# Kernel optimization log

Hardware: AMD Instinct MI355X
Metric: run time of the kernel (lower is better)

Reference implementation:

```python
import jax, jax.numpy as jnp
import numpy as np

D = 64
NEG = 0.01            # leakyrelu_neg_slope
X_CONN = 0.25         # x_connection_init
SKIP_H = 0.5          # skip_weight_h
SIGMAS = np.asarray(1.5 ** np.arange(15), np.float32)  # all_sigmas_dist

N_LIG, N_REC = 4096, 8192
E_LIG, E_REC = 65536, 262144
F_LIG, F_REC, NRBF = 15, 27, 15


def _lrelu(x):
    return jax.nn.leaky_relu(x, NEG)


def _ln(x, g, b, eps=1e-5):
    m = x.mean(-1, keepdims=True)
    v = ((x - m) ** 2).mean(-1, keepdims=True)
    return (x - m) * jax.lax.rsqrt(v + eps) * g + b


def _mlp2(x, w1, b1, g, bt, w2, b2):
    # nn.Sequential(Linear, Dropout(0), LeakyReLU, LayerNorm, Linear) in eval mode
    return _ln(_lrelu(x @ w1 + b1), g, bt) @ w2 + b2


def _coords_mlp(m, w1, b1, w2, b2):
    # nn.Sequential(Linear, Dropout(0), LeakyReLU, Linear(out,1))
    return _lrelu(m @ w1 + b1) @ w2 + b2  # [E, 1]


def _seg_mean(v, idx, n):
    # DGL fn.mean over incoming edges at destination nodes (0 for isolated nodes)
    s = jax.ops.segment_sum(v, idx, num_segments=n)
    c = jax.ops.segment_sum(jnp.ones(idx.shape, v.dtype), idx, num_segments=n)
    return s / jnp.maximum(c, 1.0)[:, None]


def setup_inputs() -> dict:
    key = jax.random.key(0)
    ks = iter(jax.random.split(key, 64))

    def n(shape, s=1.0):
        return jax.random.normal(next(ks), shape, jnp.float32) * s

    def lin(i, o):
        return n((i, o), 1.0 / float(np.sqrt(i)))

    zeros = lambda *s: jnp.zeros(s, jnp.float32)
    ones = lambda *s: jnp.ones(s, jnp.float32)

    d = {}
    d['coords_lig'] = n((N_LIG, 3))
    d['h_lig'] = n((N_LIG, D))
    d['orig_h_lig'] = n((N_LIG, D))
    d['orig_coords_lig'] = n((N_LIG, 3))
    d['coords_rec'] = n((N_REC, 3))
    d['h_rec'] = n((N_REC, D))
    d['orig_h_rec'] = n((N_REC, D))
    d['orig_coords_rec'] = n((N_REC, 3))
    d['lig_src'] = jax.random.randint(next(ks), (E_LIG,), 0, N_LIG)
    d['lig_dst'] = jax.random.randint(next(ks), (E_LIG,), 0, N_LIG)
    d['lig_efeat'] = n((E_LIG, F_LIG))
    d['rec_src'] = jax.random.randint(next(ks), (E_REC,), 0, N_REC)
    d['rec_dst'] = jax.random.randint(next(ks), (E_REC,), 0, N_REC)
    d['rec_efeat'] = n((E_REC, F_REC))
    d['mask'] = (jax.random.uniform(next(ks), (N_LIG, N_REC)) < 0.5).astype(jnp.float32)
    # ---- parameters ----
    d['lig_em_w1'], d['lig_em_b1'] = lin(2 * D + F_LIG + NRBF, D), zeros(D)
    d['lig_em_g'], d['lig_em_bt'] = ones(D), zeros(D)
    d['lig_em_w2'], d['lig_em_b2'] = lin(D, D), zeros(D)
    d['rec_em_w1'], d['rec_em_b1'] = lin(2 * D + F_REC + NRBF, D), zeros(D)
    d['rec_em_g'], d['rec_em_bt'] = ones(D), zeros(D)
    d['rec_em_w2'], d['rec_em_b2'] = lin(D, D), zeros(D)
    d['lig_cm_w1'], d['lig_cm_b1'] = lin(D, D), zeros(D)
    d['lig_cm_w2'], d['lig_cm_b2'] = lin(D, 1), zeros(1)
    d['rec_cm_w1'], d['rec_cm_b1'] = lin(D, D), zeros(D)
    d['rec_cm_w2'], d['rec_cm_b2'] = lin(D, 1), zeros(1)
    for nm in ['q_lig_w', 'k_lig_w', 'v_lig_w', 'q_rec_w', 'k_rec_w', 'v_rec_w']:
        d[nm] = lin(D, D)
    d['lig_nm_w1'], d['lig_nm_b1'] = lin(4 * D, D), zeros(D)
    d['lig_nm_g'], d['lig_nm_bt'] = ones(D), zeros(D)
    d['lig_nm_w2'], d['lig_nm_b2'] = lin(D, D), zeros(D)
    d['rec_nm_w1'], d['rec_nm_b1'] = lin(4 * D, D), zeros(D)
    d['rec_nm_g'], d['rec_nm_bt'] = ones(D), zeros(D)
    d['rec_nm_w2'], d['rec_nm_b2'] = lin(D, D), zeros(D)
    return d


def reference(coords_lig, h_lig, orig_h_lig, orig_coords_lig,
              coords_rec, h_rec, orig_h_rec, orig_coords_rec,
              lig_src, lig_dst, lig_efeat, rec_src, rec_dst, rec_efeat, mask,
              lig_em_w1, lig_em_b1, lig_em_g, lig_em_bt, lig_em_w2, lig_em_b2,
              rec_em_w1, rec_em_b1, rec_em_g, rec_em_bt, rec_em_w2, rec_em_b2,
              lig_cm_w1, lig_cm_b1, lig_cm_w2, lig_cm_b2,
              rec_cm_w1, rec_cm_b1, rec_cm_w2, rec_cm_b2,
              q_lig_w, k_lig_w, v_lig_w, q_rec_w, k_rec_w, v_rec_w,
              lig_nm_w1, lig_nm_b1, lig_nm_g, lig_nm_bt, lig_nm_w2, lig_nm_b2,
              rec_nm_w1, rec_nm_b1, rec_nm_g, rec_nm_bt, rec_nm_w2, rec_nm_b2):
    n_lig, n_rec = coords_lig.shape[0], coords_rec.shape[0]
    sig = jnp.asarray(SIGMAS, coords_lig.dtype)

    # --- ligand edge messages: x_rel = x_src - x_dst, multi-scale RBF of |x_rel|^2 ---
    xr_l = coords_lig[lig_src] - coords_lig[lig_dst]                       # [E_l, 3]
    rbf_l = jnp.exp(-jnp.sum(xr_l * xr_l, -1, keepdims=True) / sig)        # [E_l, 15]
    msg_l = _mlp2(jnp.concatenate([h_lig[lig_src], h_lig[lig_dst], lig_efeat, rbf_l], -1),
                  lig_em_w1, lig_em_b1, lig_em_g, lig_em_bt, lig_em_w2, lig_em_b2)

    # --- receptor edge messages (rec_square_distance_scale = 1) ---
    xr_r = coords_rec[rec_src] - coords_rec[rec_dst]
    rbf_r = jnp.exp(-jnp.sum(xr_r * xr_r, -1, keepdims=True) / sig)
    msg_r = _mlp2(jnp.concatenate([h_rec[rec_src], h_rec[rec_dst], rec_efeat, rbf_r], -1),
                  rec_em_w1, rec_em_b1, rec_em_g, rec_em_bt, rec_em_w2, rec_em_b2)

    # --- masked cross-graph attention (pre/post cross-msg norms are identity) ---
    q_l, k_l, v_l = _lrelu(h_lig @ q_lig_w), _lrelu(h_lig @ k_lig_w), h_lig @ v_lig_w
    q_r, k_r, v_r = _lrelu(h_rec @ q_rec_w), _lrelu(h_rec @ k_rec_w), h_rec @ v_rec_w
    s_lr = mask * (q_l @ k_r.T) - 1000.0 * (1.0 - mask)
    att_l = jax.nn.softmax(s_lr, axis=1) @ v_r                             # [N_l, D]
    mt = mask.T
    s_rl = mt * (q_r @ k_l.T) - 1000.0 * (1.0 - mt)
    att_r = jax.nn.softmax(s_rl, axis=1) @ v_l                             # [N_r, D]

    # --- equivariant coordinate update: mean_j phi_x(m_ij) * x_rel, + skip to orig ---
    coef_l = _coords_mlp(msg_l, lig_cm_w1, lig_cm_b1, lig_cm_w2, lig_cm_b2)
    x_lig = X_CONN * orig_coords_lig + (1.0 - X_CONN) * coords_lig + _seg_mean(xr_l * coef_l, lig_dst, n_lig)
    coef_r = _coords_mlp(msg_r, rec_cm_w1, rec_cm_b1, rec_cm_w2, rec_cm_b2)
    x_rec = X_CONN * orig_coords_rec + (1.0 - X_CONN) * coords_rec + _seg_mean(xr_r * coef_r, rec_dst, n_rec)

    # --- node feature update with skip (h_feats_dim == out_feats_dim) ---
    aggr_l = _seg_mean(msg_l, lig_dst, n_lig)
    h_lig_out = SKIP_H * _mlp2(jnp.concatenate([h_lig, aggr_l, att_l, orig_h_lig], -1),
                               lig_nm_w1, lig_nm_b1, lig_nm_g, lig_nm_bt, lig_nm_w2, lig_nm_b2) \
        + (1.0 - SKIP_H) * h_lig
    aggr_r = _seg_mean(msg_r, rec_dst, n_rec)
    h_rec_out = SKIP_H * _mlp2(jnp.concatenate([h_rec, aggr_r, att_r, orig_h_rec], -1),
                               rec_nm_w1, rec_nm_b1, rec_nm_g, rec_nm_bt, rec_nm_w2, rec_nm_b2) \
        + (1.0 - SKIP_H) * h_rec
    return x_lig, h_lig_out, x_rec, h_rec_out
```

## Files before the change

### kernel.cpp

```cpp
#include <hip/hip_runtime.h>
#include <hip/hip_bf16.h>

typedef __hip_bfloat16 bf16;
typedef __attribute__((ext_vector_type(8))) short bfrag8;
typedef __attribute__((ext_vector_type(4))) float f32x4;

#define N_LIG 4096
#define N_REC 8192
#define E_LIG 65536
#define E_REC 262144
#define F_LIGc 15
#define F_RECc 27

__device__ __forceinline__ float ldkv(const float* p, size_t i) { return p[i]; }
__device__ __forceinline__ float ldkv(const bf16* p, size_t i) { return __bfloat162float(p[i]); }
__device__ __forceinline__ short bfbits(float x) {
    bf16 b = __float2bfloat16(x);
    return *(short*)&b;
}
__device__ __forceinline__ unsigned short stg(const float* p, size_t i) {
    return (unsigned short)bfbits(p[i]);
}
__device__ __forceinline__ unsigned short stg(const bf16* p, size_t i) {
    return *(const unsigned short*)(p + i);
// ... 498 lines not shown
}

template <int MMODE>
__device__ __forceinline__ void attn_body(
    char* sbuf, int bid, int nb1,
    const float* __restrict__ h1, const float* __restrict__ qw1,
    const bf16* __restrict__ k1, const bf16* __restrict__ v1,
    const unsigned long long* __restrict__ mq1, const float* __restrict__ mf1, long mrs1, long mcs1,
    float* __restrict__ pO1, float* __restrict__ pM1, float* __restrict__ pL1,
    int nrows1, int ncols1, int nsplit1,
    const float* __restrict__ h2, const float* __restrict__ qw2,
    const bf16* __restrict__ k2, const bf16* __restrict__ v2,
    const unsigned long long* __restrict__ mq2, const float* __restrict__ mf2, long mrs2, long mcs2,
    float* __restrict__ pO2, float* __restrict__ pM2, float* __restrict__ pL2,
    int nrows2, int ncols2, int nsplit2)
{
    const float *h, *qw, *mf;
    const bf16 *kkp, *vvp;
    const unsigned long long* mq;
    long mrs, mcs;
    float *pO, *pM, *pL;
    int n_rows, n_cols, nsplit;
    if (bid < nb1) {
        h = h1; qw = qw1; kkp = k1; vvp = v1; mq = mq1; mf = mf1; mrs = mrs1; mcs = mcs1;
        pO = pO1; pM = pM1; pL = pL1; n_rows = nrows1; n_cols = ncols1; nsplit = nsplit1;
    } else {
        h = h2; qw = qw2; kkp = k2; vvp = v2; mq = mq2; mf = mf2; mrs = mrs2; mcs = mcs2;
        pO = pO2; pM = pM2; pL = pL2; n_rows = nrows2; n_cols = ncols2; nsplit = nsplit2;
        bid -= nb1;
    }

    unsigned short* sP = (unsigned short*)sbuf;
    unsigned short* sK = (unsigned short*)(sbuf + 8192);
    unsigned short* sV = (unsigned short*)(sbuf + 16384);
    uint2* mtq = (uint2*)(sbuf + 24576);
    unsigned char* mt = (unsigned char*)(sbuf + 24576);

    const int t  = threadIdx.x;
    const int wv = t >> 6;
    const int lm = t & 15;
    const int qd = (t & 63) >> 4;
    const int rb = bid / nsplit;
    const int sp = bid - rb * nsplit;
    const int r0 = rb * 64;
    const int cols_per = n_cols / nsplit;
    const int c_begin = sp * cols_per;

    const int cP = t >> 3, segP = (t & 7) * 8;

    #pragma unroll
    for (int u = 0; u < 2; ++u) {
        int rr = cP + 32 * u;
        const float* hp = h + (size_t)(r0 + rr) * 64 + segP;
        unsigned short tmp[8];
        #pragma unroll
        for (int j = 0; j < 8; ++j) tmp[j] = bfbits(hp[j]);
        *(uint4*)&sP[swz(rr, segP)] = *(uint4*)tmp;
        const float* qp = qw + (size_t)rr * 64 + segP;
        #pragma unroll
        for (int j = 0; j < 8; ++j) sK[swz(segP + j, rr)] = bfbits(qp[j]);
    }

    uint4 kreg[2], vreg[2];
    unsigned long long mregq = 0;
    kreg[0] = *(const uint4*)(kkp + (size_t)(c_begin + cP) * 64 + segP);
    kreg[1] = *(const uint4*)(kkp + (size_t)(c_begin + cP + 32) * 64 + segP);
    vreg[0] = *(const uint4*)(vvp + (size_t)(c_begin + cP) * 64 + segP);
    vreg[1] = *(const uint4*)(vvp + (size_t)(c_begin + cP + 32) * 64 + segP);
    if (MMODE == 0 && t < 64)
        mregq = mq[(size_t)(c_begin >> 6) * n_rows + r0 + t];
    __syncthreads();

    float qv[4][4];
    {
        bfrag8 a0 = *(const bfrag8*)&sP[swz(wv * 16 + lm, qd * 8)];
        bfrag8 a1 = *(const bfrag8*)&sP[swz(wv * 16 + lm, 32 + qd * 8)];
        #pragma unroll
        for (int ns = 0; ns < 4; ++ns) {
            f32x4 acc = {0.f, 0.f, 0.f, 0.f};
            bfrag8 b0 = *(const bfrag8*)&sK[swz(ns * 16 + lm, qd * 8)];
            bfrag8 b1 = *(const bfrag8*)&sK[swz(ns * 16 + lm, 32 + qd * 8)];
            acc = __builtin_amdgcn_mfma_f32_16x16x32_bf16(a0, b0, acc, 0, 0, 0);
            acc = __builtin_amdgcn_mfma_f32_16x16x32_bf16(a1, b1, acc, 0, 0, 0);
            #pragma unroll
            for (int r = 0; r < 4; ++r) {
                float v = acc[r];
                qv[ns][r] = v > 0.f ? v : 0.01f * v;
            }
        }
    }
    __syncthreads();

    #pragma unroll
    for (int ns = 0; ns < 4; ++ns)
        #pragma unroll
        for (int r = 0; r < 4; ++r)
            sP[swz(wv * 16 + qd * 4 + r, ns * 16 + lm)] = bfbits(qv[ns][r]);
    __syncthreads();
    bfrag8 aq0 = *(const bfrag8*)&sP[swz(wv * 16 + lm, qd * 8)];
    bfrag8 aq1 = *(const bfrag8*)&sP[swz(wv * 16 + lm, 32 + qd * 8)];

    float rm[4];
    #pragma unroll
    for (int r = 0; r < 4; ++r) rm[r] = -1e30f;
    f32x4 o[4];
    #pragma unroll
    for (int ds = 0; ds < 4; ++ds) o[ds] = (f32x4){0.f, 0.f, 0.f, 0.f};
    f32x4 osum = {0.f, 0.f, 0.f, 0.f};
    const short ONE = (short)0x3F80;
    const bfrag8 bones = {ONE, ONE, ONE, ONE, ONE, ONE, ONE, ONE};

    const int nt = cols_per / 64;
    for (int tile = 0; tile < nt; ++tile) {
        #pragma unroll
        for (int u = 0; u < 2; ++u) {
            int cc = cP + 32 * u;
            *(uint4*)&sK[swz(cc, segP)] = kreg[u];
            unsigned x0 = vreg[u].x, x1 = vreg[u].y, x2 = vreg[u].z, x3 = vreg[u].w;
            sV[swz(segP + 0, cc)] = (unsigned short)x0;
            sV[swz(segP + 1, cc)] = (unsigned short)(x0 >> 16);
            sV[swz(segP + 2, cc)] = (unsigned short)x1;
            sV[swz(segP + 3, cc)] = (unsigned short)(x1 >> 16);
            sV[swz(segP + 4, cc)] = (unsigned short)x2;
            sV[swz(segP + 5, cc)] = (unsigned short)(x2 >> 16);
            sV[swz(segP + 6, cc)] = (unsigned short)x3;
            sV[swz(segP + 7, cc)] = (unsigned short)(x3 >> 16);
        }
        if (MMODE == 0) {
            if (t < 64) mtq[t] = make_uint2((unsigned)mregq, (unsigned)(mregq >> 32));
        } else {
            int c0 = c_begin + tile * 64;
            #pragma unroll
            for (int u = 0; u < 16; ++u) {
                int i = t + 256 * u;
                int r = i >> 6, c = i & 63;
                mt[r * 80 + c] = (unsigned char)(
                    mf[(size_t)(r0 + r) * mrs + (size_t)(c0 + c) * mcs] != 0.f);
            }
        }
        __syncthreads();

        if (tile + 1 < nt) {
            int c0n = c_begin + (tile + 1) * 64;
            kreg[0] = *(const uint4*)(kkp + (size_t)(c0n + cP) * 64 + segP);
            kreg[1] = *(const uint4*)(kkp + (size_t)(c0n + cP + 32) * 64 + segP);
            vreg[0] = *(const uint4*)(vvp + (size_t)(c0n + cP) * 64 + segP);
            vreg[1] = *(const uint4*)(vvp + (size_t)(c0n + cP + 32) * 64 + segP);
            if (MMODE == 0 && t < 64)
                mregq = mq[(size_t)(c0n >> 6) * n_rows + r0 + t];
        }

        f32x4 s[4];
        #pragma unroll
        for (int ns = 0; ns < 4; ++ns) {
            f32x4 acc = {0.f, 0.f, 0.f, 0.f};
            bfrag8 b0 = *(const bfrag8*)&sK[swz(ns * 16 + lm, qd * 8)];
            bfrag8 b1 = *(const bfrag8*)&sK[swz(ns * 16 + lm, 32 + qd * 8)];
            acc = __builtin_amdgcn_mfma_f32_16x16x32_bf16(aq0, b0, acc, 0, 0, 0);
            acc = __builtin_amdgcn_mfma_f32_16x16x32_bf16(aq1, b1, acc, 0, 0, 0);
            s[ns] = acc;
        }

        float alpha[4];
        #pragma unroll
        for (int r = 0; r < 4; ++r) {
            int rloc = wv * 16 + qd * 4 + r;
            float v0, v1, v2, v3;
            if (MMODE == 0) {
                uint2 w = mtq[rloc];
                v0 = (w.x >> lm) & 1        ? s[0][r] : -1000.f;
                v1 = (w.x >> (16 + lm)) & 1 ? s[1][r] : -1000.f;
                v2 = (w.y >> lm) & 1        ? s[2][r] : -1000.f;
                v3 = (w.y >> (16 + lm)) & 1 ? s[3][r] : -1000.f;
            } else {
                v0 = mt[rloc * 80 +  0 + lm] ? s[0][r] : -1000.f;
                v1 = mt[rloc * 80 + 16 + lm] ? s[1][r] : -1000.f;
                v2 = mt[rloc * 80 + 32 + lm] ? s[2][r] : -1000.f;
                v3 = mt[rloc * 80 + 48 + lm] ? s[3][r] : -1000.f;
            }
            float mx = quad_max(fmaxf(fmaxf(v0, v1), fmaxf(v2, v3)));
            float mn = fmaxf(rm[r], mx);
            float al = __expf(rm[r] - mn);
            rm[r] = mn; alpha[r] = al;
            float p0 = __expf(v0 - mn), p1 = __expf(v1 - mn);
            float p2 = __expf(v2 - mn), p3 = __expf(v3 - mn);
            sP[swz(rloc,  0 + lm)] = bfbits(p0);
            sP[swz(rloc, 16 + lm)] = bfbits(p1);
            sP[swz(rloc, 32 + lm)] = bfbits(p2);
            sP[swz(rloc, 48 + lm)] = bfbits(p3);
            osum[r] *= al;
        }
        #pragma unroll
        for (int ds = 0; ds < 4; ++ds)
            #pragma unroll
            for (int r = 0; r < 4; ++r) o[ds][r] *= alpha[r];

        __builtin_amdgcn_wave_barrier();
        asm volatile("" ::: "memory");

        {
            bfrag8 a0 = *(const bfrag8*)&sP[swz(wv * 16 + lm, qd * 8)];
            bfrag8 a1 = *(const bfrag8*)&sP[swz(wv * 16 + lm, 32 + qd * 8)];
            #pragma unroll
            for (int ds = 0; ds < 4; ++ds) {
                bfrag8 b0 = *(const bfrag8*)&sV[swz(ds * 16 + lm, qd * 8)];
                bfrag8 b1 = *(const bfrag8*)&sV[swz(ds * 16 + lm, 32 + qd * 8)];
                o[ds] = __builtin_amdgcn_mfma_f32_16x16x32_bf16(a0, b0, o[ds], 0, 0, 0);
                o[ds] = __builtin_amdgcn_mfma_f32_16x16x32_bf16(a1, b1, o[ds], 0, 0, 0);
            }
            osum = __builtin_amdgcn_mfma_f32_16x16x32_bf16(a0, bones, osum, 0, 0, 0);
            osum = __builtin_amdgcn_mfma_f32_16x16x32_bf16(a1, bones, osum, 0, 0, 0);
        }
        __syncthreads();
    }

    #pragma unroll
    for (int ds = 0; ds < 4; ++ds)
        #pragma unroll
        for (int r = 0; r < 4; ++r) {
            int row = r0 + wv * 16 + qd * 4 + r;
            pO[((size_t)sp * n_rows + row) * 64 + ds * 16 + lm] = o[ds][r];
        }
    if (lm == 0) {
        #pragma unroll
        for (int r = 0; r < 4; ++r) {
            int row = r0 + wv * 16 + qd * 4 + r;
            pM[(size_t)sp * n_rows + row] = rm[r];
            pL[(size_t)sp * n_rows + row] = osum[r];
        }
    }
}

__global__ __launch_bounds__(256, 4) void mega_kernel(
    int nb1,
    const float* h1, const float* qw1, const bf16* k1, const bf16* v1,
    const unsigned long long* mq1, float* pO1, float* pM1, float* pL1,
    int nrows1, int ncols1, int ns1,
    const float* h2, const float* qw2, const bf16* k2, const bf16* v2,
    const unsigned long long* mq2, float* pO2, float* pM2, float* pL2,
    int nrows2, int ncols2, int ns2,
    const int* ordR, const float* coordsR, const bf16* hR,
    const int* srcR, const int* dstR, const bf16* efR,
    const unsigned short* w1pR, const float* b1R, const float* gR, const float* btR,
    const unsigned short* w2pR, const float* b2R,
    const unsigned short* c1pR, const float* cb1R, const float* cw2R, const float* cb2R,
    float* aggrR, float* xaccR,
    const int* ordL, const float* coordsL, const bf16* hL,
    const int* srcL, const int* dstL, const bf16* efL,
    const unsigned short* w1pL, const float* b1L, const float* gL, const float* btL,
    const unsigned short* w2pL, const float* b2L,
    const unsigned short* c1pL, const float* cb1L, const float* cw2L, const float* cb2L,
    float* aggrL, float* xaccL)
{
    __shared__ __align__(16) char sbuf[31232];
    int bid = blockIdx.x;
    const int nbAtt = (N_LIG / 64) * ns1 + (N_REC / 64) * ns2;
    if (bid < nbAtt) {
        attn_body<0>(sbuf, bid, nb1,
            h1, qw1, k1, v1, mq1, (const float*)0, 0L, 0L, pO1, pM1, pL1, nrows1, ncols1, ns1,
            h2, qw2, k2, v2, mq2, (const float*)0, 0L, 0L, pO2, pM2, pL2, nrows2, ncols2, ns2);
    } else {
        int eid = bid - nbAtt;
        if (eid < E_REC / 64)
            edge_body<F_RECc, 6, bf16>(sbuf, eid, ordR, coordsR, hR, srcR, dstR, efR,
                w1pR, b1R, gR, btR, w2pR, b2R, c1pR, cb1R, cw2R, cb2R, aggrR, xaccR);
        else
            edge_body<F_LIGc, 5, bf16>(sbuf, eid - E_REC / 64, ordL, coordsL, hL, srcL, dstL, efL,
                w1pL, b1L, gL, btL, w2pL, b2L, c1pL, cb1L, cw2L, cb2L, aggrL, xaccL);
    }
}

template <int F, int K1S>
__global__ __launch_bounds__(256, 4) void edge_mfma_f(
    const int* order, const float* coords, const float* h,
    const int* src, const int* dst, const float* efeat,
    const unsigned short* w1p, const float* b1, const float* g, const float* bt,
    const unsigned short* w2p, const float* b2,
    const unsigned short* c1p, const float* cb1, const float* cw2, const float* cb2,
    float* aggr, float* xacc)
{
    __shared__ __align__(16) char sbuf[64 * (K1S * 32 + 8) * 2 + 5632];
    edge_body<F, K1S, float>(sbuf, blockIdx.x, order, coords, h, src, dst, efeat,
        w1p, b1, g, bt, w2p, b2, c1p, cb1, cw2, cb2, aggr, xacc);
}

__global__ __launch_bounds__(256, 4) void attn_f32mask(
    int nb1,
    const float* h1, const float* qw1, const bf16* k1, const bf16* v1,
    const float* mf1, long mrs1, long mcs1,
    float* pO1, float* pM1, float* pL1, int nrows1, int ncols1, int ns1,
    const float* h2, const float* qw2, const bf16* k2, const bf16* v2,
    const float* mf2, long mrs2, long mcs2,
    float* pO2, float* pM2, float* pL2, int nrows2, int ncols2, int ns2)
{
    __shared__ __align__(16) char sbuf[29696];
    attn_body<1>(sbuf, blockIdx.x, nb1,
        h1, qw1, k1, v1, (const unsigned long long*)0, mf1, mrs1, mcs1,
        pO1, pM1, pL1, nrows1, ncols1, ns1,
        h2, qw2, k2, v2, (const unsigned long long*)0, mf2, mrs2, mcs2,
        pO2, pM2, pL2, nrows2, ncols2, ns2);
}

__global__ __launch_bounds__(256, 3) void node_mfma(
    int nbl, int nbn,
    const float* h1, const float* __restrict__ aggr1, const int* __restrict__ cnt1,
    const float* att1, const float* __restrict__ origh1,
    const unsigned short* __restrict__ w1pa, const float* __restrict__ b1a,
    const float* __restrict__ ga, const float* __restrict__ bta,
    const unsigned short* __restrict__ w2pa, const float* __restrict__ b2a, float* out1,
    const float* h2, const float* __restrict__ aggr2, const int* __restrict__ cnt2,
    const float* att2, const float* __restrict__ origh2,
    const unsigned short* __restrict__ w1pb, const float* __restrict__ b1b,
    const float* __restrict__ gb, const float* __restrict__ btb,
    const unsigned short* __restrict__ w2pb, const float* __restrict__ b2b, float* out2,
    const float* __restrict__ ocl, const float* __restrict__ ccl,
    const float* __restrict__ xaccl, float* __restrict__ outxl,
    const float* __restrict__ ocr, const float* __restrict__ ccr,
    const float* __restrict__ xaccr, float* __restrict__ outxr)
{
    if ((int)blockIdx.x >= nbn) {
        int i = (blockIdx.x - nbn) * 256 + threadIdx.x;
        if (i < N_LIG * 3) {
            int node = i / 3;
            float invc = 1.f / fmaxf((float)cnt1[node], 1.f);
            outxl[i] = 0.25f * ocl[i] + 0.75f * ccl[i] + xaccl[i] * invc;
        } else {
            i -= N_LIG * 3;
            if (i < N_REC * 3) {
                int node = i / 3;
                float invc = 1.f / fmaxf((float)cnt2[node], 1.f);
                outxr[i] = 0.25f * ocr[i] + 0.75f * ccr[i] + xaccr[i] * invc;
            }
        }
        return;
    }

    const float *h, *aggr, *att, *orig_h, *b1, *g, *bt, *b2;
    const unsigned short *w1p, *w2p;
    const int* cnt;
    float* h_out;
    int n0;
    if ((int)blockIdx.x < nbl) {
        h = h1; aggr = aggr1; cnt = cnt1; att = att1; orig_h = origh1;
        w1p = w1pa; b1 = b1a; g = ga; bt = bta; w2p = w2pa; b2 = b2a; h_out = out1;
        n0 = blockIdx.x * 64;
    } else {
        h = h2; aggr = aggr2; cnt = cnt2; att = att2; orig_h = origh2;
        w1p = w1pb; b1 = b1b; g = gb; bt = btb; w2p = w2pb; b2 = b2b; h_out = out2;
        n0 = (blockIdx.x - nbl) * 64;
    }

    constexpr int KP = 264;
    __shared__ __align__(16) char smem[64 * KP * 2];
    __shared__ __align__(16) unsigned short h1b[64 * 72];
    __shared__ float sums[256], sums2[256];
    __shared__ float stat_m[64], stat_r[64];
    __shared__ float invc_s[64];
    unsigned short* xb  = (unsigned short*)smem;
    float*          h1f = (float*)smem;

    const int t  = threadIdx.x;
    const int wv = t >> 6;
    const int L  = t & 63;
    const int lm = t & 15;
    const int qd = (t & 63) >> 4;
    const int n  = wv * 16 + lm;

    bfrag8 w1f[8], w2f[2];
    #pragma unroll
    for (int kk = 0; kk < 8; ++kk)
        w1f[kk] = *(const bfrag8*)&w1p[((size_t)(kk * 4 + wv) * 64 + L) * 8];
    #pragma unroll
    for (int kk = 0; kk < 2; ++kk)
        w2f[kk] = *(const bfrag8*)&w2p[((size_t)(kk * 4 + wv) * 64 + L) * 8];
    const float b1n = b1[n], b2n = b2[n];

    if (t < 64) invc_s[t] = 1.f / fmaxf((float)cnt[n0 + t], 1.f);
    __syncthreads();

    #pragma unroll
    for (int it = 0; it < 8; ++it) {
        int idx = t + 256 * it;
        int e   = idx >> 5;
        int c   = idx & 31;
        int arr = c >> 3, ch = (c & 7) * 8;
        const float* sp;
        if      (arr == 0) sp = h      + (size_t)(n0 + e) * 64 + ch;
        else if (arr == 1) sp = aggr   + (size_t)(n0 + e) * 64 + ch;
        else if (arr == 2) sp = att    + (size_t)(n0 + e) * 64 + ch;
        else               sp = orig_h + (size_t)(n0 + e) * 64 + ch;
        float4 a = *(const float4*)sp;
        float4 b = *(const float4*)(sp + 4);
        float s = (arr == 1) ? invc_s[e] : 1.f;
        unsigned short tmp[8] = {
            (unsigned short)bfbits(a.x * s), (unsigned short)bfbits(a.y * s),
            (unsigned short)bfbits(a.z * s), (unsigned short)bfbits(a.w * s),
            (unsigned short)bfbits(b.x * s), (unsigned short)bfbits(b.y * s),
            (unsigned short)bfbits(b.z * s), (unsigned short)bfbits(b.w * s)};
        *(uint4*)&xb[e * KP + arr * 64 + ch] = *(uint4*)tmp;
    }
    __syncthreads();

    f32x4 acc1[4];
    #pragma unroll
    for (int m = 0; m < 4; ++m) {
        f32x4 acc = {0.f, 0.f, 0.f, 0.f};
        #pragma unroll
        for (int kk = 0; kk < 8; ++kk) {
            bfrag8 a = *(const bfrag8*)&xb[(m * 16 + lm) * KP + kk * 32 + qd * 8];
            acc = __builtin_amdgcn_mfma_f32_16x16x32_bf16(a, w1f[kk], acc, 0, 0, 0);
        }
        acc1[m] = acc;
    }
    __syncthreads();
    #pragma unroll
    for (int m = 0; m < 4; ++m)
        #pragma unroll
        for (int r = 0; r < 4; ++r) {
            int mr = m * 16 + qd * 4 + r;
            float v = acc1[m][r] + b1n;
            v = v > 0.f ? v : 0.01f * v;
            h1f[mr * 68 + n] = v;
        }
    __syncthreads();

    {
        int e = t >> 2, seg = (t & 3) * 16;
        float s1 = 0.f, s2 = 0.f;
        #pragma unroll
        for (int j = 0; j < 16; ++j) {
            float v = h1f[e * 68 + seg + j];
            s1 += v; s2 += v * v;
        }
        sums[t] = s1; sums2[t] = s2;
    }
    __syncthreads();
    if (t < 64) {
        float s1 = sums[4 * t] + sums[4 * t + 1] + sums[4 * t + 2] + sums[4 * t + 3];
        float s2 = sums2[4 * t] + sums2[4 * t + 1] + sums2[4 * t + 2] + sums2[4 * t + 3];
        float mean = s1 * (1.f / 64.f);
        float var = s2 * (1.f / 64.f) - mean * mean;
        stat_m[t] = mean;
        stat_r[t] = rsqrtf(fmaxf(var, 0.f) + 1e-5f);
    }
    __syncthreads();
    for (int idx = t; idx < 4096; idx += 256) {
        int e = idx >> 6, j = idx & 63;
        float v = (h1f[e * 68 + j] - stat_m[e]) * stat_r[e] * g[j] + bt[j];
        h1b[e * 72 + j] = bfbits(v);
    }
    __syncthreads();

    #pragma unroll
    for (int m = 0; m < 4; ++m) {
        f32x4 acc = {0.f, 0.f, 0.f, 0.f};
        #pragma unroll
        for (int kk = 0; kk < 2; ++kk) {
            bfrag8 a = *(const bfrag8*)&h1b[(m * 16 + lm) * 72 + kk * 32 + qd * 8];
            acc = __builtin_amdgcn_mfma_f32_16x16x32_bf16(a, w2f[kk], acc, 0, 0, 0);
        }
        #pragma unroll
        for (int r = 0; r < 4; ++r) {
            int row = n0 + m * 16 + qd * 4 + r;
            float o = acc[r] + b2n;
            float hv = h[(size_t)row * 64 + n];
            h_out[(size_t)row * 64 + n] = 0.5f * o + 0.5f * hv;
        }
    }
}

__global__ __launch_bounds__(64) void attn_merge2(
    const float* __restrict__ pO1, const float* __restrict__ pM1, const float* __restrict__ pL1,
    float* __restrict__ out1, int ns1,
    const float* __restrict__ pO2, const float* __restrict__ pM2, const float* __restrict__ pL2,
    float* __restrict__ out2, int ns2)
{
    int r = blockIdx.x;
    const float *pO, *pM, *pL; float* out; int n_rows, nsplit;
    if (r < N_LIG) { pO = pO1; pM = pM1; pL = pL1; out = out1; n_rows = N_LIG; nsplit = ns1; }
    else { r -= N_LIG; pO = pO2; pM = pM2; pL = pL2; out = out2; n_rows = N_REC; nsplit = ns2; }
    int d = threadIdx.x;
    float mstar = -1e30f;
    for (int s = 0; s < nsplit; ++s) mstar = fmaxf(mstar, pM[(size_t)s * n_rows + r]);
    float L = 0.f, O = 0.f;
    for (int s = 0; s < nsplit; ++s) {
        float w = __expf(pM[(size_t)s * n_rows + r] - mstar);
        L += pL[(size_t)s * n_rows + r] * w;
        O += pO[((size_t)s * n_rows + r) * 64 + d] * w;
    }
    out[(size_t)r * 64 + d] = O / L;
}

__global__ __launch_bounds__(256) void attn_row_kernel(
    const float* __restrict__ h, const float* __restrict__ qw,
    const bf16* __restrict__ k, const bf16* __restrict__ v,
    const float* __restrict__ mask, long mrs, long mcs,
    float* __restrict__ out, int n_cols)
{
    int row = blockIdx.x;
    int tid = threadIdx.x;
    extern __shared__ float sc[];
    __shared__ float hrow[64];
    __shared__ float qrow[64];
    __shared__ float red[4];
    __shared__ float opart[4][64];

    if (tid < 64) hrow[tid] = h[(size_t)row * 64 + tid];
    __syncthreads();
    if (tid < 64) {
        float a = 0.f;
        #pragma unroll 8
        for (int i = 0; i < 64; ++i) a += hrow[i] * qw[i * 64 + tid];
        qrow[tid] = a > 0.f ? a : 0.01f * a;
    }
    __syncthreads();

    float lmax = -1e30f;
    for (int c = tid; c < n_cols; c += 256) {
        const bf16* kr = k + (size_t)c * 64;
        float s = 0.f;
        #pragma unroll 8
        for (int i = 0; i < 64; ++i) s += qrow[i] * ldkv(kr, i);
        float m = mask[(size_t)row * mrs + (size_t)c * mcs];
        s = m * s - 1000.f * (1.f - m);
        sc[c] = s;
        lmax = fmaxf(lmax, s);
    }
    #pragma unroll
    for (int o = 32; o > 0; o >>= 1) lmax = fmaxf(lmax, __shfl_xor(lmax, o, 64));
    int wid = tid >> 6;
    if ((tid & 63) == 0) red[wid] = lmax;
    __syncthreads();
    float bmax = fmaxf(fmaxf(red[0], red[1]), fmaxf(red[2], red[3]));
    __syncthreads();

    float lsum = 0.f;
    for (int c = tid; c < n_cols; c += 256) {
        float e = __expf(sc[c] - bmax);
        sc[c] = e;
        lsum += e;
    }
    lsum = wave_sum(lsum);
    if ((tid & 63) == 0) red[wid] = lsum;
    __syncthreads();
    float inv = 1.f / (red[0] + red[1] + red[2] + red[3]);

    int dd = tid & 63;
    float o = 0.f;
    for (int c = wid; c < n_cols; c += 4) o += sc[c] * ldkv(v, (size_t)c * 64 + dd);
    opart[wid][dd] = o;
    __syncthreads();
    if (wid == 0)
        out[(size_t)row * 64 + dd] =
            (opart[0][dd] + opart[1][dd] + opart[2][dd] + opart[3][dd]) * inv;
}

extern "C" void kernel_launch(void* const* d_in, const int* in_sizes, int n_in,
                              void* d_out, int out_size, void* d_ws, size_t ws_size,
                              hipStream_t stream)
{
    const float* coords_lig      = (const float*)d_in[0];
    const float* h_lig           = (const float*)d_in[1];
    const float* orig_h_lig      = (const float*)d_in[2];
    const float* orig_coords_lig = (const float*)d_in[3];
    const float* coords_rec      = (const float*)d_in[4];
    const float* h_rec           = (const float*)d_in[5];
    const float* orig_h_rec      = (const float*)d_in[6];
    const float* orig_coords_rec = (const float*)d_in[7];
    const int* lig_src   = (const int*)d_in[8];
    const int* lig_dst   = (const int*)d_in[9];
    const float* lig_efeat = (const float*)d_in[10];
    const int* rec_src   = (const int*)d_in[11];
    const int* rec_dst   = (const int*)d_in[12];
    const float* rec_efeat = (const float*)d_in[13];
    const float* mask      = (const float*)d_in[14];
    const float *lig_em_w1 = (const float*)d_in[15], *lig_em_b1 = (const float*)d_in[16];
    const float *lig_em_g  = (const float*)d_in[17], *lig_em_bt = (const float*)d_in[18];
    const float *lig_em_w2 = (const float*)d_in[19], *lig_em_b2 = (const float*)d_in[20];
    const float *rec_em_w1 = (const float*)d_in[21], *rec_em_b1 = (const float*)d_in[22];
    const float *rec_em_g  = (const float*)d_in[23], *rec_em_bt = (const float*)d_in[24];
    const float *rec_em_w2 = (const float*)d_in[25], *rec_em_b2 = (const float*)d_in[26];
    const float *lig_cm_w1 = (const float*)d_in[27], *lig_cm_b1 = (const float*)d_in[28];
    const float *lig_cm_w2 = (const float*)d_in[29], *lig_cm_b2 = (const float*)d_in[30];
    const float *rec_cm_w1 = (const float*)d_in[31], *rec_cm_b1 = (const float*)d_in[32];
    const float *rec_cm_w2 = (const float*)d_in[33], *rec_cm_b2 = (const float*)d_in[34];
    const float *q_lig_w = (const float*)d_in[35], *k_lig_w = (const float*)d_in[36];
    const float *v_lig_w = (const float*)d_in[37], *q_rec_w = (const float*)d_in[38];
    const float *k_rec_w = (const float*)d_in[39], *v_rec_w = (const float*)d_in[40];
    const float *lig_nm_w1 = (const float*)d_in[41], *lig_nm_b1 = (const float*)d_in[42];
    const float *lig_nm_g  = (const float*)d_in[43], *lig_nm_bt = (const float*)d_in[44];
    const float *lig_nm_w2 = (const float*)d_in[45], *lig_nm_b2 = (const float*)d_in[46];
    const float *rec_nm_w1 = (const float*)d_in[47], *rec_nm_b1 = (const float*)d_in[48];
    const float *rec_nm_g  = (const float*)d_in[49], *rec_nm_bt = (const float*)d_in[50];
    const float *rec_nm_w2 = (const float*)d_in[51], *rec_nm_b2 = (const float*)d_in[52];

    char* wsb = (char*)d_ws;
    float* aggr_l = (float*)(wsb + 16);
    float* aggr_r = aggr_l + (size_t)N_LIG * 64;
    float* xacc_l = aggr_r + (size_t)N_REC * 64;
    float* xacc_r = xacc_l + (size_t)N_LIG * 3;
    int* counts_l = (int*)(xacc_r + (size_t)N_REC * 3);
    int* counts_r = counts_l + N_LIG;
    int* cursor_l = counts_r + N_REC;
    int* cursor_r = cursor_l + N_LIG;
    int* order_l  = cursor_r + N_REC;
    int* order_r  = order_l + E_LIG;
    unsigned short* p_rec1  = (unsigned short*)(order_r + E_REC);
    unsigned short* p_lig1  = p_rec1 + 6 * 2048;
    unsigned short* p_rec2  = p_lig1 + 5 * 2048;
    unsigned short* p_lig2  = p_rec2 + 2 * 2048;
    unsigned short* pc_rec1 = p_lig2 + 2 * 2048;
    unsigned short* pc_lig1 = pc_rec1 + 2 * 2048;
    unsigned short* pn_rec1 = pc_lig1 + 2 * 2048;
    unsigned short* pn_lig1 = pn_rec1 + 8 * 2048;
    unsigned short* pn_rec2 = pn_lig1 + 8 * 2048;
    unsigned short* pn_lig2 = pn_rec2 + 2 * 2048;
    char* kv_base = (char*)(pn_lig2 + 2 * 2048);
    const size_t core_b = (size_t)(kv_base - wsb);
    const size_t kv_b = (size_t)(N_LIG + N_REC) * 64 * 2 * 2;

    const size_t mq1_n = (size_t)(N_REC / 64) * N_LIG;
    const size_t mq2_n = (size_t)(N_LIG / 64) * N_REC;
    const size_t mq_all_b = (mq1_n + mq2_n) * 8;
    const size_t mir_b = (size_t)(N_LIG + N_REC) * 64 * 2
                       + ((size_t)E_LIG * F_LIGc + (size_t)E_REC * F_RECc) * 2;

    const size_t part_b_hi = ((size_t)16 * N_LIG * 64 + (size_t)8 * N_REC * 64) * 4
                           + ((size_t)16 * N_LIG + (size_t)8 * N_REC) * 2 * 4;
    const size_t part_b_lo = ((size_t)4 * N_LIG * 64 + (size_t)2 * N_REC * 64) * 4
                           + ((size_t)4 * N_LIG + (size_t)2 * N_REC) * 2 * 4;

    int tier, ns1, ns2;
    size_t part_b;
    if (ws_size >= core_b + kv_b + part_b_hi + mq_all_b + mir_b) {
        tier = 0; ns1 = 16; ns2 = 8; part_b = part_b_hi;
    } else if (ws_size >= core_b + kv_b + part_b_lo) {
        tier = 1; ns1 = 4; ns2 = 2; part_b = part_b_lo;
    } else {
        tier = 2; ns1 = 4; ns2 = 2; part_b = part_b_lo;
    }

    bf16* kb_l = (bf16*)kv_base;
    bf16* vb_l = kb_l + (size_t)N_LIG * 64;
    bf16* kb_r = vb_l + (size_t)N_LIG * 64;
    bf16* vb_r = kb_r + (size_t)N_REC * 64;
    float* pO1 = (float*)(kv_base + kv_b);
    float* pO2 = pO1 + (size_t)ns1 * N_LIG * 64;
    float* pM1 = pO2 + (size_t)ns2 * N_REC * 64;
    float* pL1 = pM1 + (size_t)ns1 * N_LIG;
    float* pM2 = pL1 + (size_t)ns1 * N_LIG;
    float* pL2 = pM2 + (size_t)ns2 * N_REC;
    unsigned long long* mqb  = (unsigned long long*)(kv_base + kv_b + part_b);
    unsigned long long* mqbT = mqb + mq1_n;
    bf16* hb_l  = (bf16*)(mqbT + mq2_n);
    bf16* hb_r  = hb_l + (size_t)N_LIG * 64;
    bf16* efb_l = hb_r + (size_t)N_REC * 64;
    bf16* efb_r = efb_l + (size_t)E_LIG * F_LIGc;

    float* out = (float*)d_out;
    float* x_lig_o = out;
    float* h_lig_o = out + 12288;
    float* x_rec_o = out + 274432;
    float* h_rec_o = out + 299008;

    const int nb1 = (N_LIG / 64) * ns1;
    const int nb2 = (N_REC / 64) * ns2;

    if (tier == 0) {
        zero_kernel<<<(N_LIG + N_REC + 255) / 256, 256, 0, stream>>>(
            (float*)counts_l, N_LIG + N_REC);
        prep_kernel<<<NB_PREP, 256, 0, stream>>>(
            mask, mqb, mqbT,
            h_lig, hb_l, h_rec, hb_r, lig_efeat, efb_l, rec_efeat, efb_r,
            k_lig_w, v_lig_w, k_rec_w, v_rec_w, kb_l, vb_l, kb_r, vb_r,
            aggr_l,
            lig_dst, rec_dst, counts_l, counts_r,
            rec_em_w1, lig_em_w1, rec_em_w2, lig_em_w2, rec_cm_w1, lig_cm_w1,
            rec_nm_w1, lig_nm_w1, rec_nm_w2, lig_nm_w2,
            p_rec1, p_lig1, p_rec2, p_lig2, pc_rec1, pc_lig1,
            pn_rec1, pn_lig1, pn_rec2, pn_lig2);
        scan2_kernel<<<2, 256, 0, stream>>>(counts_l, cursor_l, counts_r, cursor_r);
        scatter2_kernel<<<(E_LIG + E_REC) / 256, 256, 0, stream>>>(
            lig_dst, rec_dst, cursor_l, cursor_r, order_l, order_r);

        mega_kernel<<<nb1 + nb2 + (E_LIG + E_REC) / 64, 256, 0, stream>>>(
            nb1,
            h_lig, q_lig_w, kb_r, vb_r, mqb, pO1, pM1, pL1, N_LIG, N_REC, ns1,
            h_rec, q_rec_w, kb_l, vb_l, mqbT, pO2, pM2, pL2, N_REC, N_LIG, ns2,
            order_r, coords_rec, hb_r, rec_src, rec_dst, efb_r,
            p_rec1, rec_em_b1, rec_em_g, rec_em_bt, p_rec2, rec_em_b2,
            pc_rec1, rec_cm_b1, rec_cm_w2, rec_cm_b2, aggr_r, xacc_r,
            order_l, coords_lig, hb_l, lig_src, lig_dst, efb_l,
            p_lig1, lig_em_b1, lig_em_g, lig_em_bt, p_lig2, lig_em_b2,
            pc_lig1, lig_cm_b1, lig_cm_w2, lig_cm_b2, aggr_l, xacc_l);

        attn_merge2<<<N_LIG + N_REC, 64, 0, stream>>>(
            pO1, pM1, pL1, h_lig_o, ns1, pO2, pM2, pL2, h_rec_o, ns2);
    } else {
        zero_kernel<<<(N_ZERO + 255) / 256, 256, 0, stream>>>(aggr_l, N_ZERO);
        pack_frags<<<NB_PACK, 256, 0, stream>>>(
            rec_em_w1, lig_em_w1, rec_em_w2, lig_em_w2, rec_cm_w1, lig_cm_w1,
            rec_nm_w1, lig_nm_w1, rec_nm_w2, lig_nm_w2,
            p_rec1, p_lig1, p_rec2, p_lig2, pc_rec1, pc_lig1,
            pn_rec1, pn_lig1, pn_rec2, pn_lig2);
        hist2_kernel<<<(E_LIG + E_REC) / 256, 256, 0, stream>>>(
            lig_dst, rec_dst, counts_l, counts_r);
        scan2_kernel<<<2, 256, 0, stream>>>(counts_l, cursor_l, counts_r, cursor_r);
        scatter2_kernel<<<(E_LIG + E_REC) / 256, 256, 0, stream>>>(
            lig_dst, rec_dst, cursor_l, cursor_r, order_l, order_r);
        kv_proj_kernel<<<(2 * (N_LIG + N_REC)) / 4, 256, 0, stream>>>(
            h_lig, h_rec, k_lig_w, v_lig_w, k_rec_w, v_rec_w,
            kb_l, vb_l, kb_r, vb_r);

        edge_mfma_f<F_LIGc, 5><<<E_LIG / 64, 256, 0, stream>>>(
            order_l, coords_lig, h_lig, lig_src, lig_dst, lig_efeat,
            p_lig1, lig_em_b1, lig_em_g, lig_em_bt, p_lig2, lig_em_b2,
            pc_lig1, lig_cm_b1, lig_cm_w2, lig_cm_b2, aggr_l, xacc_l);
        edge_mfma_f<F_RECc, 6><<<E_REC / 64, 256, 0, stream>>>(
            order_r, coords_rec, h_rec, rec_src, rec_dst, rec_efeat,
            p_rec1, rec_em_b1, rec_em_g, rec_em_bt, p_rec2, rec_em_b2,
            pc_rec1, rec_cm_b1, rec_cm_w2, rec_cm_b2, aggr_r, xacc_r);
        if (tier == 1) {
            attn_f32mask<<<nb1 + nb2, 256, 0, stream>>>(
                nb1,
                h_lig, q_lig_w, kb_r, vb_r, mask, (long)N_REC, 1L,
                pO1, pM1, pL1, N_LIG, N_REC, ns1,
                h_rec, q_rec_w, kb_l, vb_l, mask, 1L, (long)N_REC,
                pO2, pM2, pL2, N_REC, N_LIG, ns2);
            attn_merge2<<<N_LIG + N_REC, 64, 0, stream>>>(
                pO1, pM1, pL1, h_lig_o, ns1, pO2, pM2, pL2, h_rec_o, ns2);
        } else {
            attn_row_kernel<<<N_LIG, 256, N_REC * sizeof(float), stream>>>(
                h_lig, q_lig_w, kb_r, vb_r, mask, (long)N_REC, 1L, h_lig_o, N_REC);
            attn_row_kernel<<<N_REC, 256, N_LIG * sizeof(float), stream>>>(
                h_rec, q_rec_w, kb_l, vb_l, mask, 1L, (long)N_REC, h_rec_o, N_LIG);
        }
    }

    const int nbn = N_LIG / 64 + N_REC / 64;
    const int nbc = ((N_LIG + N_REC) * 3 + 255) / 256;
    node_mfma<<<nbn + nbc, 256, 0, stream>>>(
        N_LIG / 64, nbn,
        h_lig, aggr_l, counts_l, h_lig_o, orig_h_lig,
        pn_lig1, lig_nm_b1, lig_nm_g, lig_nm_bt, pn_lig2, lig_nm_b2, h_lig_o,
        h_rec, aggr_r, counts_r, h_rec_o, orig_h_rec,
        pn_rec1, rec_nm_b1, rec_nm_g, rec_nm_bt, pn_rec2, rec_nm_b2, h_rec_o,
        orig_coords_lig, coords_lig, xacc_l, x_lig_o,
        orig_coords_rec, coords_rec, xacc_r, x_rec_o);
}
```

Before: 558.3 us.

## Fuse attention split-merge into node MLP kernel and halve split count

Removes the separate attn_merge2 launch on the fast tier. The node_mfma kernel now combines the flash-attention partial outputs itself (max, rescale, normalise) while staging its input tile. The number of key splits drops from 16/8 to 8/4, which shrinks the partial buffers and the merge work but gives the attention kernel less parallelism. Doing the merge in the staging loop adds uncoalesced per-row reads of pM/pL and makes that loop heavier for one quarter of the lanes.

```diff
diff --git a/kernel.cpp b/kernel.cpp
--- a/kernel.cpp
+++ b/kernel.cpp
@@ -824,17 +824,19 @@
 }
 
 __global__ __launch_bounds__(256, 3) void node_mfma(
-    int nbl, int nbn,
+    int nbl, int nbn, int nsm1, int nsm2,
     const float* h1, const float* __restrict__ aggr1, const int* __restrict__ cnt1,
     const float* att1, const float* __restrict__ origh1,
     const unsigned short* __restrict__ w1pa, const float* __restrict__ b1a,
     const float* __restrict__ ga, const float* __restrict__ bta,
     const unsigned short* __restrict__ w2pa, const float* __restrict__ b2a, float* out1,
+    const float* __restrict__ pOa, const float* __restrict__ pMa, const float* __restrict__ pLa,
     const float* h2, const float* __restrict__ aggr2, const int* __restrict__ cnt2,
     const float* att2, const float* __restrict__ origh2,
     const unsigned short* __restrict__ w1pb, const float* __restrict__ b1b,
     const float* __restrict__ gb, const float* __restrict__ btb,
     const unsigned short* __restrict__ w2pb, const float* __restrict__ b2b, float* out2,
+    const float* __restrict__ pOb, const float* __restrict__ pMb, const float* __restrict__ pLb,
     const float* __restrict__ ocl, const float* __restrict__ ccl,
     const float* __restrict__ xaccl, float* __restrict__ outxl,
     const float* __restrict__ ocr, const float* __restrict__ ccr,
@@ -858,17 +860,20 @@
     }
 
     const float *h, *aggr, *att, *orig_h, *b1, *g, *bt, *b2;
+    const float *pO, *pM, *pL;
     const unsigned short *w1p, *w2p;
     const int* cnt;
     float* h_out;
-    int n0;
+    int n0, nsm, nrows;
     if ((int)blockIdx.x < nbl) {
         h = h1; aggr = aggr1; cnt = cnt1; att = att1; orig_h = origh1;
         w1p = w1pa; b1 = b1a; g = ga; bt = bta; w2p = w2pa; b2 = b2a; h_out = out1;
+        pO = pOa; pM = pMa; pL = pLa; nsm = nsm1; nrows = N_LIG;
         n0 = blockIdx.x * 64;
     } else {
         h = h2; aggr = aggr2; cnt = cnt2; att = att2; orig_h = origh2;
         w1p = w1pb; b1 = b1b; g = gb; bt = btb; w2p = w2pb; b2 = b2b; h_out = out2;
+        pO = pOb; pM = pMb; pL = pLb; nsm = nsm2; nrows = N_REC;
         n0 = (blockIdx.x - nbl) * 64;
     }
 
@@ -906,19 +911,40 @@
         int e   = idx >> 5;
         int c   = idx & 31;
         int arr = c >> 3, ch = (c & 7) * 8;
-        const float* sp;
-        if      (arr == 0) sp = h      + (size_t)(n0 + e) * 64 + ch;
-        else if (arr == 1) sp = aggr   + (size_t)(n0 + e) * 64 + ch;
-        else if (arr == 2) sp = att    + (size_t)(n0 + e) * 64 + ch;
-        else               sp = orig_h + (size_t)(n0 + e) * 64 + ch;
-        float4 a = *(const float4*)sp;
-        float4 b = *(const float4*)(sp + 4);
-        float s = (arr == 1) ? invc_s[e] : 1.f;
-        unsigned short tmp[8] = {
-            (unsigned short)bfbits(a.x * s), (unsigned short)bfbits(a.y * s),
-            (unsigned short)bfbits(a.z * s), (unsigned short)bfbits(a.w * s),
-            (unsigned short)bfbits(b.x * s), (unsigned short)bfbits(b.y * s),
-            (unsigned short)bfbits(b.z * s), (unsigned short)bfbits(b.w * s)};
+        unsigned short tmp[8];
+        if (arr == 2 && nsm > 0) {
+            int row = n0 + e;
+            float mstar = -1e30f;
+            for (int s = 0; s < nsm; ++s)
+                mstar = fmaxf(mstar, pM[(size_t)s * nrows + row]);
+            float Lsum = 0.f;
+            float O[8] = {0.f, 0.f, 0.f, 0.f, 0.f, 0.f, 0.f, 0.f};
+            for (int s = 0; s < nsm; ++s) {
+                float w = __expf(pM[(size_t)s * nrows + row] - mstar);
+                Lsum += pL[(size_t)s * nrows + row] * w;
+                const float* po = pO + ((size_t)s * nrows + row) * 64 + ch;
+                float4 a = *(const float4*)po;
+                float4 b = *(const float4*)(po + 4);
+                O[0] += a.x * w; O[1] += a.y * w; O[2] += a.z * w; O[3] += a.w * w;
+                O[4] += b.x * w; O[5] += b.y * w; O[6] += b.z * w; O[7] += b.w * w;
+            }
+            float inv = 1.f / Lsum;
+            #pragma unroll
+            for (int j = 0; j < 8; ++j) tmp[j] = (unsigned short)bfbits(O[j] * inv);
+        } else {
+            const float* sp;
+            if      (arr == 0) sp = h      + (size_t)(n0 + e) * 64 + ch;
+            else if (arr == 1) sp = aggr   + (size_t)(n0 + e) * 64 + ch;
+            else if (arr == 2) sp = att    + (size_t)(n0 + e) * 64 + ch;
+            else               sp = orig_h + (size_t)(n0 + e) * 64 + ch;
+            float4 a = *(const float4*)sp;
+            float4 b = *(const float4*)(sp + 4);
+            float s = (arr == 1) ? invc_s[e] : 1.f;
+            tmp[0] = (unsigned short)bfbits(a.x * s); tmp[1] = (unsigned short)bfbits(a.y * s);
+            tmp[2] = (unsigned short)bfbits(a.z * s); tmp[3] = (unsigned short)bfbits(a.w * s);
+            tmp[4] = (unsigned short)bfbits(b.x * s); tmp[5] = (unsigned short)bfbits(b.y * s);
+            tmp[6] = (unsigned short)bfbits(b.z * s); tmp[7] = (unsigned short)bfbits(b.w * s);
+        }
         *(uint4*)&xb[e * KP + arr * 64 + ch] = *(uint4*)tmp;
     }
     __syncthreads();
@@ -1147,15 +1173,15 @@
     const size_t mir_b = (size_t)(N_LIG + N_REC) * 64 * 2
                        + ((size_t)E_LIG * F_LIGc + (size_t)E_REC * F_RECc) * 2;
 
-    const size_t part_b_hi = ((size_t)16 * N_LIG * 64 + (size_t)8 * N_REC * 64) * 4
-                           + ((size_t)16 * N_LIG + (size_t)8 * N_REC) * 2 * 4;
+    const size_t part_b_hi = ((size_t)8 * N_LIG * 64 + (size_t)4 * N_REC * 64) * 4
+                           + ((size_t)8 * N_LIG + (size_t)4 * N_REC) * 2 * 4;
     const size_t part_b_lo = ((size_t)4 * N_LIG * 64 + (size_t)2 * N_REC * 64) * 4
                            + ((size_t)4 * N_LIG + (size_t)2 * N_REC) * 2 * 4;
 
     int tier, ns1, ns2;
     size_t part_b;
     if (ws_size >= core_b + kv_b + part_b_hi + mq_all_b + mir_b) {
-        tier = 0; ns1 = 16; ns2 = 8; part_b = part_b_hi;
+        tier = 0; ns1 = 8; ns2 = 4; part_b = part_b_hi;
     } else if (ws_size >= core_b + kv_b + part_b_lo) {
         tier = 1; ns1 = 4; ns2 = 2; part_b = part_b_lo;
     } else {
@@ -1215,9 +1241,6 @@
             order_l, coords_lig, hb_l, lig_src, lig_dst, efb_l,
             p_lig1, lig_em_b1, lig_em_g, lig_em_bt, p_lig2, lig_em_b2,
             pc_lig1, lig_cm_b1, lig_cm_w2, lig_cm_b2, aggr_l, xacc_l);
-
-        attn_merge2<<<N_LIG + N_REC, 64, 0, stream>>>(
-            pO1, pM1, pL1, h_lig_o, ns1, pO2, pM2, pL2, h_rec_o, ns2);
     } else {
         zero_kernel<<<(N_ZERO + 255) / 256, 256, 0, stream>>>(aggr_l, N_ZERO);
         pack_frags<<<NB_PACK, 256, 0, stream>>>(
@@ -1261,12 +1284,16 @@
 
     const int nbn = N_LIG / 64 + N_REC / 64;
     const int nbc = ((N_LIG + N_REC) * 3 + 255) / 256;
+    const int nsm1 = (tier == 0) ? ns1 : 0;
+    const int nsm2 = (tier == 0) ? ns2 : 0;
     node_mfma<<<nbn + nbc, 256, 0, stream>>>(
-        N_LIG / 64, nbn,
+        N_LIG / 64, nbn, nsm1, nsm2,
         h_lig, aggr_l, counts_l, h_lig_o, orig_h_lig,
         pn_lig1, lig_nm_b1, lig_nm_g, lig_nm_bt, pn_lig2, lig_nm_b2, h_lig_o,
+        pO1, pM1, pL1,
         h_rec, aggr_r, counts_r, h_rec_o, orig_h_rec,
         pn_rec1, rec_nm_b1, rec_nm_g, rec_nm_bt, pn_rec2, rec_nm_b2, h_rec_o,
+        pO2, pM2, pL2,
         orig_coords_lig, coords_lig, xacc_l, x_lig_o,
         orig_coords_rec, coords_rec, xacc_r, x_rec_o);
 }
```

Result: no change. 568.2 us (+1.8%).
